# Kernel tuning notes

Measured on AMD Instinct MI355X. Metric: run time of the kernel, lower is better.

Reference implementation:

```python
import jax, jax.numpy as jnp
import numpy as np

B, N, D, H, V, E, T = 128, 49, 512, 512, 10000, 512, 20


def setup_inputs() -> dict:
    key = jax.random.key(0)
    ks = jax.random.split(key, 12)
    s = 0.02  # weight init scale
    return {
        "img_features": jax.random.normal(ks[0], (B, N, D), jnp.float32),
        "captions": jax.random.randint(ks[1], (B, T), 0, V, jnp.int32),
        "embed": jax.random.normal(ks[2], (V, E), jnp.float32) * s,
        "W_v": jax.random.normal(ks[3], (D, D), jnp.float32) * s,
        "W_h": jax.random.normal(ks[4], (D, H), jnp.float32) * s,
        "att_b": jnp.zeros((N,), jnp.float32),
        "W_a": jax.random.normal(ks[5], (D,), jnp.float32) * s,
        "W_ih": jax.random.normal(ks[6], (4 * H, E + D), jnp.float32) * s,
        "b_ih": jnp.zeros((4 * H,), jnp.float32),
        "W_hh": jax.random.normal(ks[7], (4 * H, H), jnp.float32) * s,
        "b_hh": jnp.zeros((4 * H,), jnp.float32),
        "W_out": jax.random.normal(ks[8], (V, H), jnp.float32) * s,
        "b_out": jnp.zeros((V,), jnp.float32),
    }


def reference(img_features, captions, embed, W_v, W_h, att_b, W_a,
              W_ih, b_ih, W_hh, b_hh, W_out, b_out):
    b, n, d = img_features.shape
    t_len = captions.shape[1]
    h_dim = W_hh.shape[1]
    emb = embed[captions]                       # [B,T,E]
    mean_ctx = img_features.mean(axis=1)        # [B,D] (context at t=0)
    fv = jnp.einsum('bnd,ed->bne', img_features, W_v)  # precomputed W_v @ feats

    def step(carry, xs):
        h, c = carry
        emb_t, t = xs                           # emb_t: [B,E]
        # additive attention (computed for all t; masked out at t=0)
        oh = h @ W_h.T                          # [B,D]
        act = jax.nn.relu(fv + oh[:, None, :] + att_b[None, :, None])
        a = jax.nn.softmax(act @ W_a, axis=1)   # [B,N]
        z = jnp.einsum('bnd,bn->bd', img_features, a)
        context = jnp.where(t == 0, mean_ctx, z)
        alpha = jnp.where(t == 0, jnp.zeros_like(a), a)
        x = jnp.concatenate([context, emb_t], axis=1)   # [B, D+E]
        gates = x @ W_ih.T + b_ih + h @ W_hh.T + b_hh   # [B, 4H]
        i, f, g, o = jnp.split(gates, 4, axis=1)
        c = jax.nn.sigmoid(f) * c + jax.nn.sigmoid(i) * jnp.tanh(g)
        h = jax.nn.sigmoid(o) * jnp.tanh(c)
        out = h @ W_out.T + b_out               # [B,V]
        return (h, c), (out, alpha)

    h0 = jnp.zeros((b, h_dim), img_features.dtype)
    c0 = jnp.zeros((b, h_dim), img_features.dtype)
    _, (preds, alphas) = jax.lax.scan(
        step, (h0, c0), (emb.transpose(1, 0, 2), jnp.arange(t_len)))
    predictions = preds.transpose(1, 0, 2)      # [B,T,V]
    alphas = alphas.transpose(1, 2, 0)          # [B,N,T]
    return predictions, alphas
```

## Files before the change

### kernel.cpp

```cpp
#include <hip/hip_runtime.h>
#include <hip/hip_bf16.h>

#define BB 128
#define NN 49
#define VV 10000
#define TT 20

typedef short s8x8 __attribute__((ext_vector_type(8)));
typedef __bf16 bf8x8 __attribute__((ext_vector_type(8)));
typedef float f32x4 __attribute__((ext_vector_type(4)));

__device__ __forceinline__ float bf2f(short s){ return (float)__builtin_bit_cast(__bf16, s); }
__device__ __forceinline__ short f2bf(float f){ return __builtin_bit_cast(short, (__bf16)f); }

__device__ __forceinline__ s8x8 cast8(const float* p){
  float4 a = *(const float4*)p;
  float4 b = *(const float4*)(p + 4);
  s8x8 r;
  r[0] = f2bf(a.x); r[1] = f2bf(a.y); r[2] = f2bf(a.z); r[3] = f2bf(a.w);
  r[4] = f2bf(b.x); r[5] = f2bf(b.y); r[6] = f2bf(b.z); r[7] = f2bf(b.w);
  return r;
}

__device__ __forceinline__ f32x4 mfma16(s8x8 a, s8x8 b, f32x4 c){
  return __builtin_amdgcn_mfma_f32_16x16x32_bf16(
      __builtin_bit_cast(bf8x8, a), __builtin_bit_cast(bf8x8, b), c, 0, 0, 0);
}

__global__ __launch_bounds__(256) void k_prep2(
    const float* __restrict__ Whh, const float* __restrict__ Wih,
    const float* __restrict__ Wh,
    short* __restrict__ wcatp, short* __restrict__ whp)
{
  const long CW = 393216;
  const long CH = 32768;
  for (long c = blockIdx.x*256L + threadIdx.x; c < CW + CH; c += (long)gridDim.x*256L){
    if (c < CW){
      long s = c*8;
      int jt = (int)(s / 196608);
      int r  = (int)(s % 196608);
      int it = r >> 13;
      int r2 = r & 8191;
      int row = r2 >> 6, kk = r2 & 63;
      int jg = ((row>>5)<<9) + jt*32 + (row&31);
      int k = it*64 + kk;
      const float* src = (k < 512) ? (Whh + (long)jg*512 + k)
                                   : (Wih + (long)jg*1024 + (k - 512));
      *(s8x8*)(wcatp + s) = cast8(src);
    } else {
      long j = (c - CW)*8;
      *(s8x8*)(whp + j) = cast8(Wh + j);
    }
  }
}

__global__ __launch_bounds__(256) void k_packout(const float* __restrict__ Wout,
                                                 short* __restrict__ woutbf)
{
  for (long c = blockIdx.x*256L + threadIdx.x; c < 640000; c += (long)gridDim.x*256L)
    *(s8x8*)(woutbf + c*8) = cast8(Wout + c*8);
}

__global__ __launch_bounds__(256) void k_fv(const float* __restrict__ img,
    const float* __restrict__ Wv, const float* __restrict__ attb,
    short* __restrict__ fvbf)
{
  const int n0 = blockIdx.x*128, m0 = blockIdx.y*128;
  __shared__ short As[128*40];
  __shared__ short Bs[128*40];
  const int tid = threadIdx.x, w = tid>>6, lane = tid&63;
  f32x4 acc[8][2] = {};
  for (int k0 = 0; k0 < 512; k0 += 32){
    for (int c = tid; c < 512; c += 256){
      int row = c>>2, ko = (c&3)*8;
      *(s8x8*)(As + row*40 + ko) = cast8(img + (long)(m0+row)*512 + k0 + ko);
      *(s8x8*)(Bs + row*40 + ko) = cast8(Wv  + (long)(n0+row)*512 + k0 + ko);
    }
    __syncthreads();
    const int kb = (lane>>4)*8, l15 = lane&15;
    s8x8 b0f = *(const s8x8*)(Bs + (w*32 + l15)*40 + kb);
    s8x8 b1f = *(const s8x8*)(Bs + (w*32 + 16 + l15)*40 + kb);
    #pragma unroll
    for (int mt = 0; mt < 8; mt++){
      s8x8 a = *(const s8x8*)(As + (mt*16 + l15)*40 + kb);
      acc[mt][0] = mfma16(a, b0f, acc[mt][0]);
      acc[mt][1] = mfma16(a, b1f, acc[mt][1]);
    }
    __syncthreads();
  }
  const int l15 = lane&15;
  #pragma unroll
  for (int mt = 0; mt < 8; mt++){
    int rb = m0 + mt*16 + ((lane>>4)<<2);
    #pragma unroll
    for (int nt = 0; nt < 2; nt++){
      int cg = n0 + w*32 + nt*16 + l15;
      #pragma unroll
      for (int rr = 0; rr < 4; rr++){
        int r = rb + rr;
        fvbf[(long)r*512 + cg] = f2bf(acc[mt][nt][rr] + attb[r % NN]);
      }
    }
  }
}

__global__ __launch_bounds__(256) void k_att(const short* __restrict__ Hcur,
    const short* __restrict__ whp, const short* __restrict__ fvbf,
    const float* __restrict__ Wa, const float* __restrict__ img,
    short* __restrict__ Cbuf, float* __restrict__ alph, int t)
{
  const int b = blockIdx.x, tid = threadIdx.x;
  if (t == 0){
    for (int d = tid; d < 512; d += 256){
      float s = 0.f;
      for (int n = 0; n < NN; n++) s += img[((long)b*NN + n)*512 + d];
      Cbuf[b*512 + d] = f2bf(s * (1.f/49.f));
    }
    if (tid < NN) alph[((long)b*NN + tid)*TT] = 0.f;
    return;
  }
  __shared__ float hs[512];
  __shared__ float ohs[512];
  __shared__ float ee[64];
  __shared__ float zp[4][512];
  for (int d = tid; d < 512; d += 256) hs[d] = bf2f(Hcur[b*512 + d]);
  __syncthreads();
  for (int d = tid; d < 512; d += 256){
    const short* wr = whp + (long)d*512;
    float s = 0.f;
    for (int j8 = 0; j8 < 512; j8 += 8){
      s8x8 v = *(const s8x8*)(wr + j8);
      #pragma unroll
      for (int q = 0; q < 8; q++) s = fmaf(hs[j8+q], bf2f(v[q]), s);
    }
    ohs[d] = s;
  }
  __syncthreads();
  const int w = tid>>6, lane = tid&63;
  float ohr[8], war[8];
  {
    const float* wp = Wa + lane*8;
    #pragma unroll
    for (int q = 0; q < 8; q++){ ohr[q] = ohs[lane*8 + q]; war[q] = wp[q]; }
  }
  for (int n = w; n < NN; n += 4){
    s8x8 v = *(const s8x8*)(fvbf + ((long)b*NN + n)*512 + lane*8);
    float s = 0.f;
    #pragma unroll
    for (int q = 0; q < 8; q++)
      s = fmaf(fmaxf(bf2f(v[q]) + ohr[q], 0.f), war[q], s);
    #pragma unroll
    for (int off = 32; off; off >>= 1) s += __shfl_xor(s, off);
    if (lane == 0) ee[n] = s;
  }
  __syncthreads();
  if (tid < 64){
    float e = (tid < NN) ? ee[tid] : -1e30f;
    float m = e;
    #pragma unroll
    for (int off = 32; off; off >>= 1) m = fmaxf(m, __shfl_xor(m, off));
    float ex = (tid < NN) ? __expf(e - m) : 0.f;
    float s = ex;
    #pragma unroll
    for (int off = 32; off; off >>= 1) s += __shfl_xor(s, off);
    float a = ex / s;
    if (tid < NN){ ee[tid] = a; alph[((long)b*NN + tid)*TT + t] = a; }
  }
  __syncthreads();
  const int cq = tid>>6, d0 = (tid&63)*8;
  float z[8] = {0,0,0,0,0,0,0,0};
  for (int n = cq; n < NN; n += 4){
    float an = ee[n];
    const float* ip = img + ((long)b*NN + n)*512 + d0;
    float4 u0 = *(const float4*)ip;
    float4 u1 = *(const float4*)(ip + 4);
    z[0] = fmaf(an, u0.x, z[0]); z[1] = fmaf(an, u0.y, z[1]);
    z[2] = fmaf(an, u0.z, z[2]); z[3] = fmaf(an, u0.w, z[3]);
    z[4] = fmaf(an, u1.x, z[4]); z[5] = fmaf(an, u1.y, z[5]);
    z[6] = fmaf(an, u1.z, z[6]); z[7] = fmaf(an, u1.w, z[7]);
  }
  #pragma unroll
  for (int q = 0; q < 8; q++) zp[cq][d0 + q] = z[q];
  __syncthreads();
  if (tid < 64){
    int dd = tid*8;
    s8x8 o;
    #pragma unroll
    for (int q = 0; q < 8; q++)
      o[q] = f2bf(zp[0][dd+q] + zp[1][dd+q] + zp[2][dd+q] + zp[3][dd+q]);
    *(s8x8*)(Cbuf + b*512 + dd) = o;
  }
}

__global__ __launch_bounds__(256) void k_gat(const short* __restrict__ Hcur,
    const short* __restrict__ Cbuf, const short* __restrict__ wcatp,
    const float* __restrict__ embed, const int* __restrict__ caps,
    const float* __restrict__ bih, const float* __restrict__ bhh,
    float* __restrict__ cst, short* __restrict__ Hnxt,
    short* __restrict__ Hall, int t)
{
  const int jt = blockIdx.x, b0 = blockIdx.y*16;
  const int J0 = jt*32;
  __shared__ short As[16*76];
  __shared__ short Bs[128*76];
  __shared__ float gs[16][132];
  const int tid = threadIdx.x, w = tid>>6, lane = tid&63;
  const long wbase = (long)jt*24*8192;

  s8x8 a_r, b_r[4];
  auto stage_load = [&](int it){
    if (tid < 128){
      int row = tid>>3, kkc = (tid&7)*8;
      int k = it*64 + kkc, gb = b0 + row;
      s8x8 av = {0,0,0,0,0,0,0,0};
      if (k < 512){
        if (t != 0) av = *(const s8x8*)(Hcur + (long)gb*512 + k);
      } else if (k < 1024){
        av = *(const s8x8*)(Cbuf + (long)gb*512 + (k - 512));
      } else {
        av = cast8(embed + (long)caps[gb*TT + t]*512 + (k - 1024));
      }
      a_r = av;
    }
    #pragma unroll
    for (int i = 0; i < 4; i++){
      long c = tid + i*256;
      b_r[i] = *(const s8x8*)(wcatp + wbase + (long)it*8192 + c*8);
    }
  };

  f32x4 acc[2] = {};
  stage_load(0);
  for (int it = 0; it < 24; ++it){
    if (tid < 128)
      *(s8x8*)(As + (tid>>3)*76 + (tid&7)*8) = a_r;
    #pragma unroll
    for (int i = 0; i < 4; i++){
      int c = tid + i*256;
      *(s8x8*)(Bs + (c>>3)*76 + (c&7)*8) = b_r[i];
    }
    __syncthreads();
    if (it < 23) stage_load(it + 1);
    const int kb = (lane>>4)*8, l15 = lane&15, cw = w*32;
    #pragma unroll
    for (int ks = 0; ks < 2; ks++){
      s8x8 b0f = *(const s8x8*)(Bs + (cw + l15)*76 + kb + ks*32);
      s8x8 b1f = *(const s8x8*)(Bs + (cw + 16 + l15)*76 + kb + ks*32);
      s8x8 a = *(const s8x8*)(As + l15*76 + kb + ks*32);
      acc[0] = mfma16(a, b0f, acc[0]);
      acc[1] = mfma16(a, b1f, acc[1]);
    }
    __syncthreads();
  }
  {
    const int l15 = lane&15;
    int rl = (lane>>4)<<2;
    #pragma unroll
    for (int nt = 0; nt < 2; nt++){
      int ct = w*32 + nt*16 + l15;
      #pragma unroll
      for (int rr = 0; rr < 4; rr++)
        gs[rl+rr][ct] = acc[nt][rr];
    }
  }
  __syncthreads();
  for (int task = tid; task < 512; task += 256){
    int bl = task>>5, jc = task&31;
    int gb = b0 + bl, j = J0 + jc;
    float gi = gs[bl][jc]      + bih[j]        + bhh[j];
    float gf = gs[bl][32+jc]   + bih[512+j]    + bhh[512+j];
    float gg = gs[bl][64+jc]   + bih[1024+j]   + bhh[1024+j];
    float go = gs[bl][96+jc]   + bih[1536+j]   + bhh[1536+j];
    float ii = 1.f/(1.f+__expf(-gi));
    float ff = 1.f/(1.f+__expf(-gf));
    float e2 = __expf(2.f*gg); float g2 = (e2-1.f)/(e2+1.f);
    float oo = 1.f/(1.f+__expf(-go));
    float cp = (t == 0) ? 0.f : cst[gb*512 + j];
    float cN = ff*cp + ii*g2;
    float e3 = __expf(2.f*cN); float th = (e3-1.f)/(e3+1.f);
    float hN = oo*th;
    cst[gb*512 + j] = cN;
    short hb = f2bf(hN);
    Hnxt[gb*512 + j] = hb;
    Hall[((long)gb*TT + t)*512 + j] = hb;
  }
}

__global__ __launch_bounds__(256) void k_out(const short* __restrict__ Abf,
    const short* __restrict__ Bbf, float* __restrict__ outf,
    const float* __restrict__ bias)
{
  int flat = blockIdx.y*79 + blockIdx.x;
  int xcd = flat & 7, idx = flat >> 3;
  int wg = (xcd < 4) ? xcd*198 + idx : 792 + (xcd-4)*197 + idx;
  const int n0 = (wg/20)*128, m0 = (wg%20)*128;
  __shared__ short As[128*40];
  __shared__ short Bs[128*40];
  const int tid = threadIdx.x, w = tid>>6, lane = tid&63;
  f32x4 acc[8][2] = {};
  for (int k0 = 0; k0 < 512; k0 += 32){
    for (int c = tid; c < 512; c += 256){
      int row = c>>2, ko = (c&3)*8;
      int kos = ((c&3) ^ (row&3))*8;
      *(s8x8*)(As + row*40 + kos) = *(const s8x8*)(Abf + (long)(m0+row)*512 + k0 + ko);
      int brow = n0 + row;
      s8x8 bv = {0,0,0,0,0,0,0,0};
      if (brow < VV) bv = *(const s8x8*)(Bbf + (long)brow*512 + k0 + ko);
      *(s8x8*)(Bs + row*40 + kos) = bv;
    }
    __syncthreads();
    const int l15 = lane&15;
    const int kb = (((lane>>4) ^ (l15&3)))*8;
    s8x8 b0f = *(const s8x8*)(Bs + (w*32 + l15)*40 + kb);
    s8x8 b1f = *(const s8x8*)(Bs + (w*32 + 16 + l15)*40 + kb);
    #pragma unroll
    for (int mt = 0; mt < 8; mt++){
      s8x8 a = *(const s8x8*)(As + (mt*16 + l15)*40 + kb);
      acc[mt][0] = mfma16(a, b0f, acc[mt][0]);
      acc[mt][1] = mfma16(a, b1f, acc[mt][1]);
    }
    __syncthreads();
  }
  const int l15 = lane&15;
  #pragma unroll
  for (int mt = 0; mt < 8; mt++){
    int rb = m0 + mt*16 + ((lane>>4)<<2);
    #pragma unroll
    for (int nt = 0; nt < 2; nt++){
      int cg = n0 + w*32 + nt*16 + l15;
      if (cg >= VV) continue;
      #pragma unroll
      for (int rr = 0; rr < 4; rr++){
        int r = rb + rr;
        outf[(long)r*VV + cg] = acc[mt][nt][rr] + bias[cg];
      }
    }
  }
}

extern "C" void kernel_launch(void* const* d_in, const int* in_sizes, int n_in,
                              void* d_out, int out_size, void* d_ws, size_t ws_size,
                              hipStream_t stream)
{
  const float* img  = (const float*)d_in[0];
  const int*   caps = (const int*)d_in[1];
  const float* emb  = (const float*)d_in[2];
  const float* Wv   = (const float*)d_in[3];
  const float* Wh   = (const float*)d_in[4];
  const float* attb = (const float*)d_in[5];
  const float* Wa   = (const float*)d_in[6];
  const float* Wih  = (const float*)d_in[7];
  const float* bih  = (const float*)d_in[8];
  const float* Whh  = (const float*)d_in[9];
  const float* bhh  = (const float*)d_in[10];
  const float* Wout = (const float*)d_in[11];
  const float* bout = (const float*)d_in[12];
  float* preds = (float*)d_out;
  float* alph  = preds + (long)BB*TT*VV;

  char* ws = (char*)d_ws;
  short* wcatp  = (short*)(ws);
  short* whp    = (short*)(ws + 6291456);
  short* fvbf   = (short*)(ws + 6815744);
  short* Hbuf   = (short*)(ws + 13238272);
  short* Cbuf   = (short*)(ws + 13500416);
  float* cst    = (float*)(ws + 13631488);
  short* Hall   = (short*)(ws + 13893632);
  short* woutbf = (short*)(ws);

  k_prep2<<<1024, 256, 0, stream>>>(Whh, Wih, Wh, wcatp, whp);
  k_fv<<<dim3(4,49), 256, 0, stream>>>(img, Wv, attb, fvbf);

  for (int t = 0; t < TT; t++){
    short* Hc = Hbuf + (t&1)*65536;
    short* Hn = Hbuf + ((t+1)&1)*65536;
    k_att<<<128, 256, 0, stream>>>(Hc, whp, fvbf, Wa, img, Cbuf, alph, t);
    k_gat<<<dim3(16,8), 256, 0, stream>>>(Hc, Cbuf, wcatp, emb, caps, bih, bhh,
                                          cst, Hn, Hall, t);
  }

  k_packout<<<1024, 256, 0, stream>>>(Wout, woutbf);
  k_out<<<dim3(79,20), 256, 0, stream>>>(Hall, woutbf, preds, bout);
}
```

Before: 974.1 us.

## Fuse recurrent loop into one persistent kernel with software grid barriers

Replaces the 40 per-timestep launches of the attention and gate kernels with a single persistent 128-block kernel that loops over timesteps and uses an atomic-counter grid barrier between phases. This is meant to remove kernel launch and drain overhead on the serial recurrence. It relies on all 128 blocks being co-resident, otherwise the barrier deadlocks. The change also removes the XOR swizzle from the output GEMM's shared-memory tiles, which may bring back LDS bank conflicts.

```diff
diff --git a/kernel.cpp b/kernel.cpp
--- a/kernel.cpp
+++ b/kernel.cpp
@@ -25,6 +25,24 @@
 __device__ __forceinline__ f32x4 mfma16(s8x8 a, s8x8 b, f32x4 c){
   return __builtin_amdgcn_mfma_f32_16x16x32_bf16(
       __builtin_bit_cast(bf8x8, a), __builtin_bit_cast(bf8x8, b), c, 0, 0, 0);
+}
+
+__device__ __forceinline__ void grid_bar(unsigned* bar, int nblk){
+  __syncthreads();
+  if (threadIdx.x == 0){
+    __threadfence();
+    unsigned g = __hip_atomic_load(bar + 1, __ATOMIC_RELAXED, __HIP_MEMORY_SCOPE_AGENT);
+    unsigned a = __hip_atomic_fetch_add(bar, 1u, __ATOMIC_ACQ_REL, __HIP_MEMORY_SCOPE_AGENT);
+    if (a == (unsigned)(nblk - 1)){
+      __hip_atomic_store(bar, 0u, __ATOMIC_RELAXED, __HIP_MEMORY_SCOPE_AGENT);
+      __hip_atomic_fetch_add(bar + 1, 1u, __ATOMIC_RELEASE, __HIP_MEMORY_SCOPE_AGENT);
+    } else {
+      while (__hip_atomic_load(bar + 1, __ATOMIC_ACQUIRE, __HIP_MEMORY_SCOPE_AGENT) == g)
+        __builtin_amdgcn_s_sleep(2);
+    }
+    __threadfence();
+  }
+  __syncthreads();
 }
 
 __global__ __launch_bounds__(256) void k_prep2(
@@ -104,185 +122,194 @@
   }
 }
 
-__global__ __launch_bounds__(256) void k_att(const short* __restrict__ Hcur,
+__global__ __launch_bounds__(256) void k_loop(
     const short* __restrict__ whp, const short* __restrict__ fvbf,
     const float* __restrict__ Wa, const float* __restrict__ img,
-    short* __restrict__ Cbuf, float* __restrict__ alph, int t)
-{
-  const int b = blockIdx.x, tid = threadIdx.x;
-  if (t == 0){
-    for (int d = tid; d < 512; d += 256){
-      float s = 0.f;
-      for (int n = 0; n < NN; n++) s += img[((long)b*NN + n)*512 + d];
-      Cbuf[b*512 + d] = f2bf(s * (1.f/49.f));
-    }
-    if (tid < NN) alph[((long)b*NN + tid)*TT] = 0.f;
-    return;
-  }
+    const short* __restrict__ wcatp, const float* __restrict__ embed,
+    const int* __restrict__ caps, const float* __restrict__ bih,
+    const float* __restrict__ bhh, short* __restrict__ Hbuf,
+    short* __restrict__ Cbuf, float* __restrict__ cst,
+    short* __restrict__ Hall, float* __restrict__ alph,
+    unsigned* __restrict__ bar)
+{
   __shared__ float hs[512];
   __shared__ float ohs[512];
   __shared__ float ee[64];
   __shared__ float zp[4][512];
-  for (int d = tid; d < 512; d += 256) hs[d] = bf2f(Hcur[b*512 + d]);
-  __syncthreads();
-  for (int d = tid; d < 512; d += 256){
-    const short* wr = whp + (long)d*512;
-    float s = 0.f;
-    for (int j8 = 0; j8 < 512; j8 += 8){
-      s8x8 v = *(const s8x8*)(wr + j8);
-      #pragma unroll
-      for (int q = 0; q < 8; q++) s = fmaf(hs[j8+q], bf2f(v[q]), s);
-    }
-    ohs[d] = s;
-  }
-  __syncthreads();
-  const int w = tid>>6, lane = tid&63;
-  float ohr[8], war[8];
-  {
-    const float* wp = Wa + lane*8;
-    #pragma unroll
-    for (int q = 0; q < 8; q++){ ohr[q] = ohs[lane*8 + q]; war[q] = wp[q]; }
-  }
-  for (int n = w; n < NN; n += 4){
-    s8x8 v = *(const s8x8*)(fvbf + ((long)b*NN + n)*512 + lane*8);
-    float s = 0.f;
-    #pragma unroll
-    for (int q = 0; q < 8; q++)
-      s = fmaf(fmaxf(bf2f(v[q]) + ohr[q], 0.f), war[q], s);
-    #pragma unroll
-    for (int off = 32; off; off >>= 1) s += __shfl_xor(s, off);
-    if (lane == 0) ee[n] = s;
-  }
-  __syncthreads();
-  if (tid < 64){
-    float e = (tid < NN) ? ee[tid] : -1e30f;
-    float m = e;
-    #pragma unroll
-    for (int off = 32; off; off >>= 1) m = fmaxf(m, __shfl_xor(m, off));
-    float ex = (tid < NN) ? __expf(e - m) : 0.f;
-    float s = ex;
-    #pragma unroll
-    for (int off = 32; off; off >>= 1) s += __shfl_xor(s, off);
-    float a = ex / s;
-    if (tid < NN){ ee[tid] = a; alph[((long)b*NN + tid)*TT + t] = a; }
-  }
-  __syncthreads();
-  const int cq = tid>>6, d0 = (tid&63)*8;
-  float z[8] = {0,0,0,0,0,0,0,0};
-  for (int n = cq; n < NN; n += 4){
-    float an = ee[n];
-    const float* ip = img + ((long)b*NN + n)*512 + d0;
-    float4 u0 = *(const float4*)ip;
-    float4 u1 = *(const float4*)(ip + 4);
-    z[0] = fmaf(an, u0.x, z[0]); z[1] = fmaf(an, u0.y, z[1]);
-    z[2] = fmaf(an, u0.z, z[2]); z[3] = fmaf(an, u0.w, z[3]);
-    z[4] = fmaf(an, u1.x, z[4]); z[5] = fmaf(an, u1.y, z[5]);
-    z[6] = fmaf(an, u1.z, z[6]); z[7] = fmaf(an, u1.w, z[7]);
-  }
-  #pragma unroll
-  for (int q = 0; q < 8; q++) zp[cq][d0 + q] = z[q];
-  __syncthreads();
-  if (tid < 64){
-    int dd = tid*8;
-    s8x8 o;
-    #pragma unroll
-    for (int q = 0; q < 8; q++)
-      o[q] = f2bf(zp[0][dd+q] + zp[1][dd+q] + zp[2][dd+q] + zp[3][dd+q]);
-    *(s8x8*)(Cbuf + b*512 + dd) = o;
-  }
-}
-
-__global__ __launch_bounds__(256) void k_gat(const short* __restrict__ Hcur,
-    const short* __restrict__ Cbuf, const short* __restrict__ wcatp,
-    const float* __restrict__ embed, const int* __restrict__ caps,
-    const float* __restrict__ bih, const float* __restrict__ bhh,
-    float* __restrict__ cst, short* __restrict__ Hnxt,
-    short* __restrict__ Hall, int t)
-{
-  const int jt = blockIdx.x, b0 = blockIdx.y*16;
-  const int J0 = jt*32;
   __shared__ short As[16*76];
   __shared__ short Bs[128*76];
   __shared__ float gs[16][132];
-  const int tid = threadIdx.x, w = tid>>6, lane = tid&63;
-  const long wbase = (long)jt*24*8192;
-
-  s8x8 a_r, b_r[4];
-  auto stage_load = [&](int it){
-    if (tid < 128){
-      int row = tid>>3, kkc = (tid&7)*8;
-      int k = it*64 + kkc, gb = b0 + row;
-      s8x8 av = {0,0,0,0,0,0,0,0};
-      if (k < 512){
-        if (t != 0) av = *(const s8x8*)(Hcur + (long)gb*512 + k);
-      } else if (k < 1024){
-        av = *(const s8x8*)(Cbuf + (long)gb*512 + (k - 512));
+
+  const int bid = blockIdx.x, tid = threadIdx.x;
+  const int w = tid>>6, lane = tid&63;
+
+  for (int t = 0; t < TT; t++){
+    const short* Hcur = Hbuf + (t&1)*65536;
+    short*       Hnxt = Hbuf + ((t+1)&1)*65536;
+
+    {
+      const int b = bid;
+      if (t == 0){
+        for (int d = tid; d < 512; d += 256){
+          float s = 0.f;
+          for (int n = 0; n < NN; n++) s += img[((long)b*NN + n)*512 + d];
+          Cbuf[b*512 + d] = f2bf(s * (1.f/49.f));
+        }
+        if (tid < NN) alph[((long)b*NN + tid)*TT] = 0.f;
       } else {
-        av = cast8(embed + (long)caps[gb*TT + t]*512 + (k - 1024));
-      }
-      a_r = av;
-    }
-    #pragma unroll
-    for (int i = 0; i < 4; i++){
-      long c = tid + i*256;
-      b_r[i] = *(const s8x8*)(wcatp + wbase + (long)it*8192 + c*8);
-    }
-  };
-
-  f32x4 acc[2] = {};
-  stage_load(0);
-  for (int it = 0; it < 24; ++it){
-    if (tid < 128)
-      *(s8x8*)(As + (tid>>3)*76 + (tid&7)*8) = a_r;
-    #pragma unroll
-    for (int i = 0; i < 4; i++){
-      int c = tid + i*256;
-      *(s8x8*)(Bs + (c>>3)*76 + (c&7)*8) = b_r[i];
-    }
-    __syncthreads();
-    if (it < 23) stage_load(it + 1);
-    const int kb = (lane>>4)*8, l15 = lane&15, cw = w*32;
-    #pragma unroll
-    for (int ks = 0; ks < 2; ks++){
-      s8x8 b0f = *(const s8x8*)(Bs + (cw + l15)*76 + kb + ks*32);
-      s8x8 b1f = *(const s8x8*)(Bs + (cw + 16 + l15)*76 + kb + ks*32);
-      s8x8 a = *(const s8x8*)(As + l15*76 + kb + ks*32);
-      acc[0] = mfma16(a, b0f, acc[0]);
-      acc[1] = mfma16(a, b1f, acc[1]);
-    }
-    __syncthreads();
-  }
-  {
-    const int l15 = lane&15;
-    int rl = (lane>>4)<<2;
-    #pragma unroll
-    for (int nt = 0; nt < 2; nt++){
-      int ct = w*32 + nt*16 + l15;
-      #pragma unroll
-      for (int rr = 0; rr < 4; rr++)
-        gs[rl+rr][ct] = acc[nt][rr];
-    }
-  }
-  __syncthreads();
-  for (int task = tid; task < 512; task += 256){
-    int bl = task>>5, jc = task&31;
-    int gb = b0 + bl, j = J0 + jc;
-    float gi = gs[bl][jc]      + bih[j]        + bhh[j];
-    float gf = gs[bl][32+jc]   + bih[512+j]    + bhh[512+j];
-    float gg = gs[bl][64+jc]   + bih[1024+j]   + bhh[1024+j];
-    float go = gs[bl][96+jc]   + bih[1536+j]   + bhh[1536+j];
-    float ii = 1.f/(1.f+__expf(-gi));
-    float ff = 1.f/(1.f+__expf(-gf));
-    float e2 = __expf(2.f*gg); float g2 = (e2-1.f)/(e2+1.f);
-    float oo = 1.f/(1.f+__expf(-go));
-    float cp = (t == 0) ? 0.f : cst[gb*512 + j];
-    float cN = ff*cp + ii*g2;
-    float e3 = __expf(2.f*cN); float th = (e3-1.f)/(e3+1.f);
-    float hN = oo*th;
-    cst[gb*512 + j] = cN;
-    short hb = f2bf(hN);
-    Hnxt[gb*512 + j] = hb;
-    Hall[((long)gb*TT + t)*512 + j] = hb;
+        for (int d = tid; d < 512; d += 256) hs[d] = bf2f(Hcur[b*512 + d]);
+        __syncthreads();
+        for (int d = tid; d < 512; d += 256){
+          const short* wr = whp + (long)d*512;
+          float s = 0.f;
+          for (int j8 = 0; j8 < 512; j8 += 8){
+            s8x8 v = *(const s8x8*)(wr + j8);
+            #pragma unroll
+            for (int q = 0; q < 8; q++) s = fmaf(hs[j8+q], bf2f(v[q]), s);
+          }
+          ohs[d] = s;
+        }
+        __syncthreads();
+        float ohr[8], war[8];
+        {
+          const float* wp = Wa + lane*8;
+          #pragma unroll
+          for (int q = 0; q < 8; q++){ ohr[q] = ohs[lane*8 + q]; war[q] = wp[q]; }
+        }
+        for (int n = w; n < NN; n += 4){
+          s8x8 v = *(const s8x8*)(fvbf + ((long)b*NN + n)*512 + lane*8);
+          float s = 0.f;
+          #pragma unroll
+          for (int q = 0; q < 8; q++)
+            s = fmaf(fmaxf(bf2f(v[q]) + ohr[q], 0.f), war[q], s);
+          #pragma unroll
+          for (int off = 32; off; off >>= 1) s += __shfl_xor(s, off);
+          if (lane == 0) ee[n] = s;
+        }
+        __syncthreads();
+        if (tid < 64){
+          float e = (tid < NN) ? ee[tid] : -1e30f;
+          float m = e;
+          #pragma unroll
+          for (int off = 32; off; off >>= 1) m = fmaxf(m, __shfl_xor(m, off));
+          float ex = (tid < NN) ? __expf(e - m) : 0.f;
+          float s = ex;
+          #pragma unroll
+          for (int off = 32; off; off >>= 1) s += __shfl_xor(s, off);
+          float a = ex / s;
+          if (tid < NN){ ee[tid] = a; alph[((long)b*NN + tid)*TT + t] = a; }
+        }
+        __syncthreads();
+        const int cq = tid>>6, d0 = (tid&63)*8;
+        float z[8] = {0,0,0,0,0,0,0,0};
+        for (int n = cq; n < NN; n += 4){
+          float an = ee[n];
+          const float* ip = img + ((long)b*NN + n)*512 + d0;
+          float4 u0 = *(const float4*)ip;
+          float4 u1 = *(const float4*)(ip + 4);
+          z[0] = fmaf(an, u0.x, z[0]); z[1] = fmaf(an, u0.y, z[1]);
+          z[2] = fmaf(an, u0.z, z[2]); z[3] = fmaf(an, u0.w, z[3]);
+          z[4] = fmaf(an, u1.x, z[4]); z[5] = fmaf(an, u1.y, z[5]);
+          z[6] = fmaf(an, u1.z, z[6]); z[7] = fmaf(an, u1.w, z[7]);
+        }
+        #pragma unroll
+        for (int q = 0; q < 8; q++) zp[cq][d0 + q] = z[q];
+        __syncthreads();
+        if (tid < 64){
+          int dd = tid*8;
+          s8x8 o;
+          #pragma unroll
+          for (int q = 0; q < 8; q++)
+            o[q] = f2bf(zp[0][dd+q] + zp[1][dd+q] + zp[2][dd+q] + zp[3][dd+q]);
+          *(s8x8*)(Cbuf + b*512 + dd) = o;
+        }
+      }
+    }
+    grid_bar(bar, 128);
+
+    {
+      const int jt = bid >> 3, b0 = (bid & 7)*16;
+      const int J0 = jt*32;
+      const long wbase = (long)jt*24*8192;
+      s8x8 a_r, b_r[4];
+      auto stage_load = [&](int it){
+        if (tid < 128){
+          int row = tid>>3, kkc = (tid&7)*8;
+          int k = it*64 + kkc, gb = b0 + row;
+          s8x8 av = {0,0,0,0,0,0,0,0};
+          if (k < 512){
+            if (t != 0) av = *(const s8x8*)(Hcur + (long)gb*512 + k);
+          } else if (k < 1024){
+            av = *(const s8x8*)(Cbuf + (long)gb*512 + (k - 512));
+          } else {
+            av = cast8(embed + (long)caps[gb*TT + t]*512 + (k - 1024));
+          }
+          a_r = av;
+        }
+        #pragma unroll
+        for (int i = 0; i < 4; i++){
+          long c = tid + i*256;
+          b_r[i] = *(const s8x8*)(wcatp + wbase + (long)it*8192 + c*8);
+        }
+      };
+
+      f32x4 acc[2] = {};
+      stage_load(0);
+      for (int it = 0; it < 24; ++it){
+        if (tid < 128)
+          *(s8x8*)(As + (tid>>3)*76 + (tid&7)*8) = a_r;
+        #pragma unroll
+        for (int i = 0; i < 4; i++){
+          int c = tid + i*256;
+          *(s8x8*)(Bs + (c>>3)*76 + (c&7)*8) = b_r[i];
+        }
+        __syncthreads();
+        if (it < 23) stage_load(it + 1);
+        const int kb = (lane>>4)*8, l15 = lane&15, cw = w*32;
+        #pragma unroll
+        for (int ks = 0; ks < 2; ks++){
+          s8x8 b0f = *(const s8x8*)(Bs + (cw + l15)*76 + kb + ks*32);
+          s8x8 b1f = *(const s8x8*)(Bs + (cw + 16 + l15)*76 + kb + ks*32);
+          s8x8 a = *(const s8x8*)(As + l15*76 + kb + ks*32);
+          acc[0] = mfma16(a, b0f, acc[0]);
+          acc[1] = mfma16(a, b1f, acc[1]);
+        }
+        __syncthreads();
+      }
+      {
+        const int l15 = lane&15;
+        int rl = (lane>>4)<<2;
+        #pragma unroll
+        for (int nt = 0; nt < 2; nt++){
+          int ct = w*32 + nt*16 + l15;
+          #pragma unroll
+          for (int rr = 0; rr < 4; rr++)
+            gs[rl+rr][ct] = acc[nt][rr];
+        }
+      }
+      __syncthreads();
+      for (int task = tid; task < 512; task += 256){
+        int bl = task>>5, jc = task&31;
+        int gb = b0 + bl, j = J0 + jc;
+        float gi = gs[bl][jc]      + bih[j]        + bhh[j];
+        float gf = gs[bl][32+jc]   + bih[512+j]    + bhh[512+j];
+        float gg = gs[bl][64+jc]   + bih[1024+j]   + bhh[1024+j];
+        float go = gs[bl][96+jc]   + bih[1536+j]   + bhh[1536+j];
+        float ii = 1.f/(1.f+__expf(-gi));
+        float ff = 1.f/(1.f+__expf(-gf));
+        float e2 = __expf(2.f*gg); float g2 = (e2-1.f)/(e2+1.f);
+        float oo = 1.f/(1.f+__expf(-go));
+        float cp = (t == 0) ? 0.f : cst[gb*512 + j];
+        float cN = ff*cp + ii*g2;
+        float e3 = __expf(2.f*cN); float th = (e3-1.f)/(e3+1.f);
+        float hN = oo*th;
+        cst[gb*512 + j] = cN;
+        short hb = f2bf(hN);
+        Hnxt[gb*512 + j] = hb;
+        Hall[((long)gb*TT + t)*512 + j] = hb;
+      }
+    }
+    grid_bar(bar, 128);
   }
 }
 
@@ -301,16 +328,14 @@
   for (int k0 = 0; k0 < 512; k0 += 32){
     for (int c = tid; c < 512; c += 256){
       int row = c>>2, ko = (c&3)*8;
-      int kos = ((c&3) ^ (row&3))*8;
-      *(s8x8*)(As + row*40 + kos) = *(const s8x8*)(Abf + (long)(m0+row)*512 + k0 + ko);
+      *(s8x8*)(As + row*40 + ko) = *(const s8x8*)(Abf + (long)(m0+row)*512 + k0 + ko);
       int brow = n0 + row;
       s8x8 bv = {0,0,0,0,0,0,0,0};
       if (brow < VV) bv = *(const s8x8*)(Bbf + (long)brow*512 + k0 + ko);
-      *(s8x8*)(Bs + row*40 + kos) = bv;
+      *(s8x8*)(Bs + row*40 + ko) = bv;
     }
     __syncthreads();
-    const int l15 = lane&15;
-    const int kb = (((lane>>4) ^ (l15&3)))*8;
+    const int kb = (lane>>4)*8, l15 = lane&15;
     s8x8 b0f = *(const s8x8*)(Bs + (w*32 + l15)*40 + kb);
     s8x8 b1f = *(const s8x8*)(Bs + (w*32 + 16 + l15)*40 + kb);
     #pragma unroll
@@ -366,18 +391,15 @@
   short* Cbuf   = (short*)(ws + 13500416);
   float* cst    = (float*)(ws + 13631488);
   short* Hall   = (short*)(ws + 13893632);
+  unsigned* bar = (unsigned*)(ws + 16515072);
   short* woutbf = (short*)(ws);
 
+  hipMemsetAsync(bar, 0, 256, stream);
   k_prep2<<<1024, 256, 0, stream>>>(Whh, Wih, Wh, wcatp, whp);
   k_fv<<<dim3(4,49), 256, 0, stream>>>(img, Wv, attb, fvbf);
 
-  for (int t = 0; t < TT; t++){
-    short* Hc = Hbuf + (t&1)*65536;
-    short* Hn = Hbuf + ((t+1)&1)*65536;
-    k_att<<<128, 256, 0, stream>>>(Hc, whp, fvbf, Wa, img, Cbuf, alph, t);
-    k_gat<<<dim3(16,8), 256, 0, stream>>>(Hc, Cbuf, wcatp, emb, caps, bih, bhh,
-                                          cst, Hn, Hall, t);
-  }
+  k_loop<<<128, 256, 0, stream>>>(whp, fvbf, Wa, img, wcatp, emb, caps,
+                                  bih, bhh, Hbuf, Cbuf, cst, Hall, alph, bar);
 
   k_packout<<<1024, 256, 0, stream>>>(Wout, woutbf);
   k_out<<<dim3(79,20), 256, 0, stream>>>(Hall, woutbf, preds, bout);
```

New measurement: 1.546 ms. 1.59x slower.
